# Performance work log

Measured on AMD Instinct MI355X. Metric: run time of the kernel, lower is better.

## Reference

```python
import jax, jax.numpy as jnp
import numpy as np
from jax import lax

BATCH = 2
COUNT = 5
OUT = 125


def _bins(n, out=OUT):
    # PyTorch adaptive_max_pool2d bin boundaries: start=floor(i*n/out), end=ceil((i+1)*n/out)
    i = np.arange(out)
    s = (i * n) // out
    e = -((-(i + 1) * n) // out)
    m = int((e - s).max())
    idx = s[:, None] + np.arange(m)[None, :]
    return np.minimum(idx, n - 1), idx < e[:, None]


def _apool(img):
    # adaptive max pool 2d of [H,W] -> [OUT,OUT]; H,W are concrete Python ints
    H, W = img.shape
    ri, rv = _bins(H)
    ci, cv = _bins(W)
    r = jnp.where(rv[:, :, None], img[ri], -jnp.inf).max(axis=1)       # [OUT, W]
    return jnp.where(cv[None], r[:, ci], -jnp.inf).max(axis=2)         # [OUT, OUT]


def _conv(x, w, b):
    y = lax.conv_general_dilated(x, w, (1, 1), 'VALID', dimension_numbers=('NCHW', 'OIHW', 'NCHW'))
    return y + b[None, :, None, None]


def _bn(x, g, be, m, v):
    inv = g * lax.rsqrt(v + 1e-5)
    return x * inv[None, :, None, None] + (be - m * inv)[None, :, None, None]


def _pool(x, k, s):
    return lax.reduce_window(x, -np.inf, lax.max, (1, 1, k, k), (1, 1, s, s), 'VALID')


def _forward(x, ROI, roi_layer, w1, b1, g1, be1, m1, v1, w2, b2, g2, be2, m2, v2,
             w3, b3, g3, be3, m3, v3, w4, b4, g4, be4, m4, v4, fw1, fb1, fw2, fb2, fw3, fb3):
    ROI = np.asarray(ROI)
    rl = int(roi_layer)
    roiX = jax.nn.relu(_bn(_conv(x, w1, b1), g1, be1, m1, v1))  # [2,3,252,252]
    crops = []
    for k in range(BATCH):
        xs = []
        for j in range(rl):
            for i in range(COUNT):
                y1, y2, x1, x2 = (int(v) for v in ROI[k, i, 0])
                y1 = int(y1 * 0.9); y2 = int(y2 * 0.9); x2 = int(x2 * 0.9); x1 = int(x1 * 0.9)
                xs.append(_apool(roiX[k, j, y1:y2, x1:x2]))
        crops.append(xs)
    # original code prepends each batch's crop list -> batch order reversed; .numpy() detaches grads
    xb = lax.stop_gradient(jnp.stack(crops[1] + crops[0]).reshape(BATCH, COUNT * rl, OUT, OUT))
    norX = _pool(jax.nn.relu(_bn(_conv(x, w2, b2), g2, be2, m2, v2)), 4, 2)  # [2,20,125,125]
    h = jnp.concatenate([norX, xb], axis=1)                                   # [2,35,125,125]
    h = _pool(jax.nn.relu(_bn(_conv(h, w3, b3), g3, be3, m3, v3)), 2, 2)      # [2,50,60,60]
    h = _pool(jax.nn.relu(_bn(_conv(h, w4, b4), g4, be4, m4, v4)), 2, 2)      # [2,25,28,28]
    h = h.reshape(BATCH, -1)                                                  # [2,19600]
    h = jax.nn.relu(h @ fw1 + fb1)
    h = jax.nn.relu(h @ fw2 + fb2)
    h = jax.nn.relu(h @ fw3 + fb3)
    return jax.nn.softmax(h, axis=1)


def setup_inputs() -> dict:
    key = jax.random.key(0)
    ks = jax.random.split(key, 8)
    rng = np.random.default_rng(0)
    y1 = rng.integers(0, 100, (BATCH, COUNT))
    y2 = np.minimum(y1 + rng.integers(60, 150, (BATCH, COUNT)), 251)
    x1 = rng.integers(0, 100, (BATCH, COUNT))
    x2 = np.minimum(x1 + rng.integers(60, 150, (BATCH, COUNT)), 251)
    ROI = jnp.asarray(np.stack([y1, y2, x1, x2], -1)[:, :, None, :].astype(np.int32))
    d = {'x': jax.random.normal(ks[0], (BATCH, 1, 256, 256), jnp.float32), 'ROI': ROI, 'roi_layer': 3}
    d.update(w1=jax.random.normal(ks[1], (3, 1, 5, 5)) * 0.05, b1=jnp.zeros(3), g1=jnp.ones(3), be1=jnp.zeros(3), m1=jnp.zeros(3), v1=jnp.ones(3))
    d.update(w2=jax.random.normal(ks[2], (20, 1, 5, 5)) * 0.05, b2=jnp.zeros(20), g2=jnp.ones(20), be2=jnp.zeros(20), m2=jnp.zeros(20), v2=jnp.ones(20))
    d.update(w3=jax.random.normal(ks[3], (50, 35, 5, 5)) * 0.05, b3=jnp.zeros(50), g3=jnp.ones(50), be3=jnp.zeros(50), m3=jnp.zeros(50), v3=jnp.ones(50))
    d.update(w4=jax.random.normal(ks[4], (25, 50, 5, 5)) * 0.05, b4=jnp.zeros(25), g4=jnp.ones(25), be4=jnp.zeros(25), m4=jnp.zeros(25), v4=jnp.ones(25))
    d.update(fw1=jax.random.normal(ks[5], (25 * 28 * 28, 1024)) * 0.01, fb1=jnp.zeros(1024),
             fw2=jax.random.normal(ks[6], (1024, 32)) * 0.05, fb2=jnp.zeros(32),
             fw3=jax.random.normal(ks[7], (32, 2)) * 0.05, fb3=jnp.zeros(2))
    return d


def reference(x, ROI, roi_layer, w1, b1, g1, be1, m1, v1, w2, b2, g2, be2, m2, v2,
              w3, b3, g3, be3, m3, v3, w4, b4, g4, be4, m4, v4, fw1, fb1, fw2, fb2, fw3, fb3):
    return _forward(x, ROI, roi_layer, w1, b1, g1, be1, m1, v1, w2, b2, g2, be2, m2, v2,
                    w3, b3, g3, be3, m3, v3, w4, b4, g4, be4, m4, v4, fw1, fb1, fw2, fb2, fw3, fb3)
```

## Files before the change

### kernel.cpp

```cpp
#include <hip/hip_runtime.h>
#include <math.h>


#define RL 3
#define NCH 35

__global__ __launch_bounds__(256) void conv2_roi(
    const float* __restrict__ x, const int* __restrict__ ROI,
    const float* __restrict__ w2, const float* __restrict__ b2, const float* __restrict__ g2,
    const float* __restrict__ be2, const float* __restrict__ m2, const float* __restrict__ v2,
    const float* __restrict__ w1, const float* __restrict__ b1, const float* __restrict__ g1,
    const float* __restrict__ be1, const float* __restrict__ m1, const float* __restrict__ v1,
    const float* __restrict__ w3, const float* __restrict__ w4,
    float* __restrict__ wp3, float* __restrict__ wp4,
    float* __restrict__ h1) {
    if (blockIdx.y >= 70) {
        const float* src = (blockIdx.y == 70) ? w3 : w4;
        float* dst = (blockIdx.y == 70) ? wp3 : wp4;
        int rows = (blockIdx.y == 70) ? 50 * 35 : 25 * 50;
        int total = rows * 28;
        for (int i = blockIdx.x * 256 + threadIdx.x; i < total; i += gridDim.x * 256) {
            int t = i % 28, r = i / 28;
            dst[i] = (t < 25) ? src[r * 25 + t] : 0.f;
        }
        return;
    }
    int i = blockIdx.x * 256 + threadIdx.x;
    if (i >= 125 * 125) return;
    int oy = i / 125, ox = i % 125;
    if (blockIdx.y < 40) {
        int c = blockIdx.y % 20;
        int bi = blockIdx.y / 20;
        const float* xp = x + bi * 256 * 256 + (2 * oy) * 256 + 2 * ox;
        float wl[25];
#pragma unroll
        for (int k = 0; k < 25; k++) wl[k] = w2[c * 25 + k];
        float in[8][8];
#pragma unroll
        for (int r = 0; r < 8; r++)
#pragma unroll
            for (int k = 0; k < 4; k++) {
                float2 v2v = *(const float2*)(xp + r * 256 + 2 * k);
                in[r][2 * k] = v2v.x;
                in[r][2 * k + 1] = v2v.y;
            }
        float inv = g2[c] * rsqrtf(v2[c] + 1e-5f);
        float sh = (b2[c] - m2[c]) * inv + be2[c];
        float mx = -INFINITY;
#pragma unroll
        for (int py = 0; py < 4; py++) {
#pragma unroll
            for (int px = 0; px < 4; px++) {
                float acc = 0.f;
#pragma unroll
                for (int ky = 0; ky < 5; ky++)
#pragma unroll
                    for (int kx = 0; kx < 5; kx++)
                        acc = fmaf(in[py + ky][px + kx], wl[ky * 5 + kx], acc);
                mx = fmaxf(mx, fmaxf(acc * inv + sh, 0.f));
            }
        }
        h1[((bi * NCH + c) * 125 + oy) * 125 + ox] = mx;
    } else {
        int yz = blockIdx.y - 40;
        int bi = yz / 15;
        int cc = yz % 15;
        int sb = 1 - bi;
        int j = cc / 5;
        int ri = cc % 5;
        const int* rp = ROI + (sb * 5 + ri) * 4;
        int y1 = (9 * rp[0]) / 10;
        int y2 = (9 * rp[1]) / 10;
        int x1 = (9 * rp[2]) / 10;
        int x2 = (9 * rp[3]) / 10;
        int H = y2 - y1;
        int W = x2 - x1;
        int sy = (oy * H) / 125, ey = ((oy + 1) * H + 124) / 125;
        int sx = (ox * W) / 125, ex = ((ox + 1) * W + 124) / 125;
        float wl[25];
#pragma unroll
        for (int k = 0; k < 25; k++) wl[k] = w1[j * 25 + k];
        float inv = g1[j] * rsqrtf(v1[j] + 1e-5f);
        float sh = (b1[j] - m1[j]) * inv + be1[j];
        const float* xp = x + sb * 256 * 256;
        float mx = -INFINITY;
        for (int r = sy; r < ey; r++) {
            for (int c2 = sx; c2 < ex; c2++) {
                int Y = y1 + r, X = x1 + c2;
                float acc = 0.f;
#pragma unroll
                for (int ky = 0; ky < 5; ky++)
#pragma unroll
                    for (int kx = 0; kx < 5; kx++)
                        acc = fmaf(xp[(Y + ky) * 256 + X + kx], wl[ky * 5 + kx], acc);
                mx = fmaxf(mx, fmaxf(acc * inv + sh, 0.f));
            }
        }
        h1[((bi * NCH + 20 + cc) * 125 + oy) * 125 + ox] = mx;
    }
}

template <int IW, int PO, int CI, int CO, int G, int NG, int NS, int BST, int CST>
__global__ __launch_bounds__(64, 4) void conv_partial(
    const float* __restrict__ in, const float* __restrict__ wp,
    float* __restrict__ pac) {
    static_assert(G == 2 || G == 3, "schedule supports G=2,3");
    __shared__ float tile[2][20][24];

    const int lane = threadIdx.x;
    const int sy = lane >> 3, sx = lane & 7;
    int z = blockIdx.z;
    const int ng = z % NG; z /= NG;
    const int s = z % NS;
    const int bi = z / NS;
    const int co0 = ng * G;
    constexpr int CPS = (CI + NS - 1) / NS;
    const int ci0 = s * CPS;
    const int ci1 = (ci0 + CPS < CI) ? ci0 + CPS : CI;
    const int px0 = (8 * (int)blockIdx.x < PO - 8) ? 8 * (int)blockIdx.x : PO - 8;
    const int py0 = (8 * (int)blockIdx.y < PO - 8) ? 8 * (int)blockIdx.y : PO - 8;
    const int px = px0 + sx, py = py0 + sy;
    const float* ip = in + (size_t)bi * BST + (size_t)(2 * py0) * IW + 2 * px0;

    int cw[G];
#pragma unroll
    for (int gg = 0; gg < G; gg++) cw[gg] = (co0 + gg < CO) ? co0 + gg : CO - 1;

    float2 sreg[4];
    auto loadstage = [&](int ci) {
        const float* src = ip + (size_t)ci * CST;
#pragma unroll
        for (int k = 0; k < 4; k++) {
            int p = lane + k * 64;
            if (p < 200) {
                int r = p / 10, c2 = (p % 10) * 2;
                sreg[k] = *(const float2*)(src + r * IW + c2);
            }
        }
    };
    auto writestage = [&](int buf) {
#pragma unroll
        for (int k = 0; k < 4; k++) {
            int p = lane + k * 64;
            if (p < 200) {
                int r = p / 10, c2 = (p % 10) * 2;
                *(float2*)&tile[buf][r][c2] = sreg[k];
            }
        }
    };

    float4 wA[7], wB[7];
    auto wload = [&](float4(&wr)[7], int gg, int ci) {
        const float* src = wp + ((size_t)cw[gg] * CI + ci) * 28;
#pragma unroll
        for (int k = 0; k < 7; k++) wr[k] = *(const float4*)(src + 4 * k);
    };

    float acc[G][4];
#pragma unroll
    for (int gg = 0; gg < G; gg++)
#pragma unroll
        for (int q = 0; q < 4; q++) acc[gg][q] = 0.f;

#define WE(W, t) ((t) % 4 == 0 ? W[(t) / 4].x : (t) % 4 == 1 ? W[(t) / 4].y : (t) % 4 == 2 ? W[(t) / 4].z : W[(t) / 4].w)
#define FMAG(W, gg)                                                            \
    {                                                                          \
        _Pragma("unroll") for (int ky = 0; ky < 5; ky++) {                     \
            _Pragma("unroll") for (int kx = 0; kx < 5; kx++) {                 \
                float wv = WE(W, ky * 5 + kx);                                 \
                float e00 = ((kx)&1) ? p[ky][kx >> 1].y : p[ky][kx >> 1].x;    \
                float e01 = ((kx + 1) & 1) ? p[ky][(kx + 1) >> 1].y : p[ky][(kx + 1) >> 1].x; \
                float e10 = ((kx)&1) ? p[ky + 1][kx >> 1].y : p[ky + 1][kx >> 1].x; \
                float e11 = ((kx + 1) & 1) ? p[ky + 1][(kx + 1) >> 1].y : p[ky + 1][(kx + 1) >> 1].x; \
                acc[gg][0] = fmaf(e00, wv, acc[gg][0]);                        \
                acc[gg][1] = fmaf(e01, wv, acc[gg][1]);                        \
                acc[gg][2] = fmaf(e10, wv, acc[gg][2]);                        \
                acc[gg][3] = fmaf(e11, wv, acc[gg][3]);                        \
            }                                                                  \
        }                                                                      \
    }

    loadstage(ci0);
    writestage(0);

    for (int ci = ci0; ci < ci1; ci++) {
        const int cur = (ci - ci0) & 1;
        if (ci + 1 < ci1) loadstage(ci + 1);
        wload(wA, 0, ci);
        float2 p[6][3];
#pragma unroll
        for (int r = 0; r < 6; r++)
#pragma unroll
            for (int c = 0; c < 3; c++)
                p[r][c] = *(const float2*)&tile[cur][2 * sy + r][2 * sx + 2 * c];
        wload(wB, 1, ci);
        FMAG(wA, 0);
        if constexpr (G == 3) {
            wload(wA, 2, ci);
            FMAG(wB, 1);
            FMAG(wA, 2);
        } else {
            FMAG(wB, 1);
        }
        if (ci + 1 < ci1) writestage(cur ^ 1);
    }
#undef FMAG
#undef WE

    constexpr int CW = 2 * PO;
#pragma unroll
    for (int gg = 0; gg < G; gg++) {
        int co = co0 + gg;
        if (co < CO) {
            size_t base = (((size_t)(s * 2 + bi) * CO + co) * CW + 2 * py) * CW + 2 * px;
            float2 r0 = {acc[gg][0], acc[gg][1]};
            float2 r1 = {acc[gg][2], acc[gg][3]};
            *(float2*)&pac[base] = r0;
            *(float2*)&pac[base + CW] = r1;
        }
    }
}

template <int PO, int CO, int INIT>
__global__ __launch_bounds__(256) void conv_finish(
    const float* __restrict__ pac,
    const float* __restrict__ b, const float* __restrict__ g,
    const float* __restrict__ be, const float* __restrict__ m,
    const float* __restrict__ v, float* __restrict__ out,
    const float* __restrict__ fb1, float* __restrict__ fc1o) {
    int idx = blockIdx.x * 256 + threadIdx.x;
    if (INIT && idx < 2048) fc1o[idx] = fb1[idx & 1023];
    int total = 2 * CO * PO * PO;
    if (idx >= total) return;
    int px = idx % PO;
    int t = idx / PO;
    int py = t % PO; t /= PO;
    int co = t % CO;
    int bi = t / CO;
    constexpr int CW = 2 * PO;
    constexpr size_t SS = (size_t)2 * CO * CW * CW;
    size_t base = (((size_t)bi * CO + co) * CW + 2 * py) * CW + 2 * px;
    float s00 = 0.f, s01 = 0.f, s10 = 0.f, s11 = 0.f;
#pragma unroll
    for (int s = 0; s < 4; s++) {
        float2 a0 = *(const float2*)&pac[base + s * SS];
        float2 a1 = *(const float2*)&pac[base + s * SS + CW];
        s00 += a0.x; s01 += a0.y; s10 += a1.x; s11 += a1.y;
    }
    float inv = g[co] * rsqrtf(v[co] + 1e-5f);
    float sh = (b[co] - m[co]) * inv + be[co];
    float q0 = fmaxf(s00 * inv + sh, 0.f);
    float q1 = fmaxf(s01 * inv + sh, 0.f);
    float q2 = fmaxf(s10 * inv + sh, 0.f);
    float q3 = fmaxf(s11 * inv + sh, 0.f);
    out[idx] = fmaxf(fmaxf(q0, q1), fmaxf(q2, q3));
}

#define CHUNK 50
__global__ void fc1_mm(const float* __restrict__ pac,
                       const float* __restrict__ b4, const float* __restrict__ g4,
                       const float* __restrict__ be4, const float* __restrict__ m4,
                       const float* __restrict__ v4,
                       const float* __restrict__ w, float* __restrict__ out) {
    __shared__ float sh[2][CHUNK];
    int o = blockIdx.x * 256 + threadIdx.x;
    int i0 = blockIdx.y * CHUNK;
    if (threadIdx.x < 2 * CHUNK) {
        int r = threadIdx.x / CHUNK, t = threadIdx.x % CHUNK;
        int e = i0 + t;
        int px = e % 28;
        int t2 = e / 28;
        int py = t2 % 28;
        int co = t2 / 28;
        const int CW = 56;
        const int SS = 2 * 25 * CW * CW;
        int base = ((r * 25 + co) * CW + 2 * py) * CW + 2 * px;
        float s00 = 0.f, s01 = 0.f, s10 = 0.f, s11 = 0.f;
#pragma unroll
        for (int s = 0; s < 4; s++) {
            float2 a0 = *(const float2*)&pac[base + s * SS];
            float2 a1 = *(const float2*)&pac[base + s * SS + CW];
            s00 += a0.x; s01 += a0.y; s10 += a1.x; s11 += a1.y;
        }
        float inv = g4[co] * rsqrtf(v4[co] + 1e-5f);
        float shv = (b4[co] - m4[co]) * inv + be4[co];
        float q0 = fmaxf(s00 * inv + shv, 0.f);
        float q1 = fmaxf(s01 * inv + shv, 0.f);
        float q2 = fmaxf(s10 * inv + shv, 0.f);
        float q3 = fmaxf(s11 * inv + shv, 0.f);
        sh[r][t] = fmaxf(fmaxf(q0, q1), fmaxf(q2, q3));
    }
    __syncthreads();
    float a0 = 0.f, a1 = 0.f;
    const float* wp = w + (size_t)i0 * 1024 + o;
#pragma unroll
    for (int i = 0; i < CHUNK; i++) {
        float wv = wp[(size_t)i * 1024];
        a0 = fmaf(sh[0][i], wv, a0);
        a1 = fmaf(sh[1][i], wv, a1);
    }
    atomicAdd(&out[o], a0);
    atomicAdd(&out[1024 + o], a1);
}

__global__ void head(const float* __restrict__ fc1o, const float* __restrict__ fw2,
                     const float* __restrict__ fb2, const float* __restrict__ fw3,
                     const float* __restrict__ fb3, float* __restrict__ out) {
    int bi = blockIdx.x;
    __shared__ float h[1024];
    __shared__ float red[256];
    __shared__ float s2[32];
    for (int i = threadIdx.x; i < 1024; i += 256) h[i] = fmaxf(fc1o[bi * 1024 + i], 0.f);
    __syncthreads();
    int o = threadIdx.x >> 3;
    int part = threadIdx.x & 7;
    float a = 0.f;
    for (int i = part * 128; i < part * 128 + 128; i++) a += h[i] * fw2[i * 32 + o];
    red[threadIdx.x] = a;
    __syncthreads();
    if (part == 0) {
        float s = 0.f;
        for (int p = 0; p < 8; p++) s += red[(o << 3) + p];
        s2[o] = fmaxf(s + fb2[o], 0.f);
    }
    __syncthreads();
    if (threadIdx.x == 0) {
        float z0 = fb3[0], z1 = fb3[1];
        for (int i = 0; i < 32; i++) {
            z0 += s2[i] * fw3[i * 2];
            z1 += s2[i] * fw3[i * 2 + 1];
        }
        z0 = fmaxf(z0, 0.f);
        z1 = fmaxf(z1, 0.f);
        float mx = fmaxf(z0, z1);
        float e0 = expf(z0 - mx), e1 = expf(z1 - mx);
        float s = e0 + e1;
        out[bi * 2 + 0] = e0 / s;
        out[bi * 2 + 1] = e1 / s;
    }
}

extern "C" void kernel_launch(void* const* d_in, const int* in_sizes, int n_in,
                              void* d_out, int out_size, void* d_ws, size_t ws_size,
                              hipStream_t stream) {
    const float* x   = (const float*)d_in[0];
    const int*   ROI = (const int*)d_in[1];
    const float* w1 = (const float*)d_in[3];
    const float* b1 = (const float*)d_in[4];
    const float* g1 = (const float*)d_in[5];
    const float* be1 = (const float*)d_in[6];
    const float* m1 = (const float*)d_in[7];
    const float* v1 = (const float*)d_in[8];
    const float* w2 = (const float*)d_in[9];
    const float* b2 = (const float*)d_in[10];
    const float* g2 = (const float*)d_in[11];
    const float* be2 = (const float*)d_in[12];
    const float* m2 = (const float*)d_in[13];
    const float* v2 = (const float*)d_in[14];
    const float* w3 = (const float*)d_in[15];
    const float* b3 = (const float*)d_in[16];
    const float* g3 = (const float*)d_in[17];
    const float* be3 = (const float*)d_in[18];
    const float* m3 = (const float*)d_in[19];
    const float* v3 = (const float*)d_in[20];
    const float* w4 = (const float*)d_in[21];
    const float* b4 = (const float*)d_in[22];
    const float* g4 = (const float*)d_in[23];
    const float* be4 = (const float*)d_in[24];
    const float* m4 = (const float*)d_in[25];
    const float* v4 = (const float*)d_in[26];
    const float* fw1 = (const float*)d_in[27];
    const float* fb1 = (const float*)d_in[28];
    const float* fw2 = (const float*)d_in[29];
    const float* fb2 = (const float*)d_in[30];
    const float* fw3 = (const float*)d_in[31];
    const float* fb3 = (const float*)d_in[32];
    float* out = (float*)d_out;

    float* ws = (float*)d_ws;
    float* h1   = ws;
    float* p3   = h1 + 1093750;
    float* fc1o = p3 + 360000;
    float* pac3 = fc1o + 2048;
    float* pac4 = pac3;
    float* wp3  = pac3 + 5760000;
    float* wp4  = wp3 + 49000;

    {
        dim3 grd((125 * 125 + 255) / 256, 72);
        conv2_roi<<<grd, 256, 0, stream>>>(x, ROI, w2, b2, g2, be2, m2, v2,
                                           w1, b1, g1, be1, m1, v1,
                                           w3, w4, wp3, wp4, h1);
    }
    {
        dim3 grd(8, 8, 2 * 4 * 17);
        conv_partial<125, 60, NCH, 50, 3, 17, 4, 35 * 15625, 15625>
            <<<grd, 64, 0, stream>>>(h1, wp3, pac3);
    }
    {
        int total = 2 * 50 * 60 * 60;
        conv_finish<60, 50, 1><<<(total + 255) / 256, 256, 0, stream>>>(
            pac3, b3, g3, be3, m3, v3, p3, fb1, fc1o);
    }
    {
        dim3 grd(4, 4, 2 * 4 * 13);
        conv_partial<60, 28, 50, 25, 2, 13, 4, 180000, 3600>
            <<<grd, 64, 0, stream>>>(p3, wp4, pac4);
    }
    {
        dim3 grd(4, 392);
        fc1_mm<<<grd, 256, 0, stream>>>(pac4, b4, g4, be4, m4, v4, fw1, fc1o);
    }
    head<<<2, 256, 0, stream>>>(fc1o, fw2, fb2, fw3, fb3, out);
}
```

Before: 118.8 us.

## Fuse MLP head into fc1 via last-block counter and vectorize fc1 loads

The separate head kernel is folded into fc1_mm. The last block to finish, found with an atomic counter that conv_finish resets, runs the fc2/fc3/softmax tail, which saves one kernel launch. fc1 is reworked so that each block covers 28 input rows across all 1024 outputs, reading weights as float4, with 700 blocks in place of a 4x392 grid. The conv_partial loop also moves the shared-memory stage write earlier so it overlaps the FMAs. The costs are more atomics per thread and a serialized tail in one block.

Result: slower. 246.8 us (+107.8%).

```diff
diff --git a/kernel.cpp b/kernel.cpp
--- a/kernel.cpp
+++ b/kernel.cpp
@@ -198,11 +198,12 @@
         if constexpr (G == 3) {
             wload(wA, 2, ci);
             FMAG(wB, 1);
+            if (ci + 1 < ci1) writestage(cur ^ 1);
             FMAG(wA, 2);
         } else {
+            if (ci + 1 < ci1) writestage(cur ^ 1);
             FMAG(wB, 1);
         }
-        if (ci + 1 < ci1) writestage(cur ^ 1);
     }
 #undef FMAG
 #undef WE
@@ -227,9 +228,10 @@
     const float* __restrict__ b, const float* __restrict__ g,
     const float* __restrict__ be, const float* __restrict__ m,
     const float* __restrict__ v, float* __restrict__ out,
-    const float* __restrict__ fb1, float* __restrict__ fc1o) {
+    const float* __restrict__ fb1, float* __restrict__ fc1o, int* __restrict__ cnt) {
     int idx = blockIdx.x * 256 + threadIdx.x;
     if (INIT && idx < 2048) fc1o[idx] = fb1[idx & 1023];
+    if (INIT && idx == 2048) *cnt = 0;
     int total = 2 * CO * PO * PO;
     if (idx >= total) return;
     int px = idx % PO;
@@ -256,17 +258,26 @@
     out[idx] = fmaxf(fmaxf(q0, q1), fmaxf(q2, q3));
 }
 
-#define CHUNK 50
-__global__ void fc1_mm(const float* __restrict__ pac,
-                       const float* __restrict__ b4, const float* __restrict__ g4,
-                       const float* __restrict__ be4, const float* __restrict__ m4,
-                       const float* __restrict__ v4,
-                       const float* __restrict__ w, float* __restrict__ out) {
+#define CHUNK 28
+#define NCHK 700
+__global__ __launch_bounds__(256) void fc1_mm(
+    const float* __restrict__ pac,
+    const float* __restrict__ b4, const float* __restrict__ g4,
+    const float* __restrict__ be4, const float* __restrict__ m4,
+    const float* __restrict__ v4,
+    const float* __restrict__ w, float* __restrict__ fc1o, int* __restrict__ cnt,
+    const float* __restrict__ fw2, const float* __restrict__ fb2,
+    const float* __restrict__ fw3, const float* __restrict__ fb3,
+    float* __restrict__ out) {
     __shared__ float sh[2][CHUNK];
-    int o = blockIdx.x * 256 + threadIdx.x;
-    int i0 = blockIdx.y * CHUNK;
-    if (threadIdx.x < 2 * CHUNK) {
-        int r = threadIdx.x / CHUNK, t = threadIdx.x % CHUNK;
+    __shared__ float hh[1024];
+    __shared__ float red[256];
+    __shared__ float s2v[32];
+    __shared__ int lastf;
+    const int tid = threadIdx.x;
+    const int i0 = blockIdx.x * CHUNK;
+    if (tid < 2 * CHUNK) {
+        int r = tid / CHUNK, t = tid % CHUNK;
         int e = i0 + t;
         int px = e % 28;
         int t2 = e / 28;
@@ -291,52 +302,67 @@
         sh[r][t] = fmaxf(fmaxf(q0, q1), fmaxf(q2, q3));
     }
     __syncthreads();
-    float a0 = 0.f, a1 = 0.f;
-    const float* wp = w + (size_t)i0 * 1024 + o;
-#pragma unroll
+    const int o4 = tid * 4;
+    float4 a0 = {0.f, 0.f, 0.f, 0.f}, a1 = {0.f, 0.f, 0.f, 0.f};
+    const float* wp = w + (size_t)i0 * 1024 + o4;
+#pragma unroll 4
     for (int i = 0; i < CHUNK; i++) {
-        float wv = wp[(size_t)i * 1024];
-        a0 = fmaf(sh[0][i], wv, a0);
-        a1 = fmaf(sh[1][i], wv, a1);
-    }
-    atomicAdd(&out[o], a0);
-    atomicAdd(&out[1024 + o], a1);
-}
-
-__global__ void head(const float* __restrict__ fc1o, const float* __restrict__ fw2,
-                     const float* __restrict__ fb2, const float* __restrict__ fw3,
-                     const float* __restrict__ fb3, float* __restrict__ out) {
-    int bi = blockIdx.x;
-    __shared__ float h[1024];
-    __shared__ float red[256];
-    __shared__ float s2[32];
-    for (int i = threadIdx.x; i < 1024; i += 256) h[i] = fmaxf(fc1o[bi * 1024 + i], 0.f);
+        float4 wv = *(const float4*)(wp + (size_t)i * 1024);
+        float h0 = sh[0][i], h1v = sh[1][i];
+        a0.x = fmaf(h0, wv.x, a0.x);
+        a0.y = fmaf(h0, wv.y, a0.y);
+        a0.z = fmaf(h0, wv.z, a0.z);
+        a0.w = fmaf(h0, wv.w, a0.w);
+        a1.x = fmaf(h1v, wv.x, a1.x);
+        a1.y = fmaf(h1v, wv.y, a1.y);
+        a1.z = fmaf(h1v, wv.z, a1.z);
+        a1.w = fmaf(h1v, wv.w, a1.w);
+    }
+    atomicAdd(&fc1o[o4 + 0], a0.x);
+    atomicAdd(&fc1o[o4 + 1], a0.y);
+    atomicAdd(&fc1o[o4 + 2], a0.z);
+    atomicAdd(&fc1o[o4 + 3], a0.w);
+    atomicAdd(&fc1o[1024 + o4 + 0], a1.x);
+    atomicAdd(&fc1o[1024 + o4 + 1], a1.y);
+    atomicAdd(&fc1o[1024 + o4 + 2], a1.z);
+    atomicAdd(&fc1o[1024 + o4 + 3], a1.w);
+
+    __threadfence();
     __syncthreads();
-    int o = threadIdx.x >> 3;
-    int part = threadIdx.x & 7;
-    float a = 0.f;
-    for (int i = part * 128; i < part * 128 + 128; i++) a += h[i] * fw2[i * 32 + o];
-    red[threadIdx.x] = a;
+    if (tid == 0) lastf = (atomicAdd(cnt, 1) == NCHK - 1) ? 1 : 0;
     __syncthreads();
-    if (part == 0) {
-        float s = 0.f;
-        for (int p = 0; p < 8; p++) s += red[(o << 3) + p];
-        s2[o] = fmaxf(s + fb2[o], 0.f);
-    }
-    __syncthreads();
-    if (threadIdx.x == 0) {
-        float z0 = fb3[0], z1 = fb3[1];
-        for (int i = 0; i < 32; i++) {
-            z0 += s2[i] * fw3[i * 2];
-            z1 += s2[i] * fw3[i * 2 + 1];
-        }
-        z0 = fmaxf(z0, 0.f);
-        z1 = fmaxf(z1, 0.f);
-        float mx = fmaxf(z0, z1);
-        float e0 = expf(z0 - mx), e1 = expf(z1 - mx);
-        float s = e0 + e1;
-        out[bi * 2 + 0] = e0 / s;
-        out[bi * 2 + 1] = e1 / s;
+    if (!lastf) return;
+    for (int bi = 0; bi < 2; bi++) {
+        for (int i = tid; i < 1024; i += 256)
+            hh[i] = fmaxf(atomicAdd(&fc1o[bi * 1024 + i], 0.f), 0.f);
+        __syncthreads();
+        int o = tid >> 3;
+        int part = tid & 7;
+        float a = 0.f;
+        for (int i = part * 128; i < part * 128 + 128; i++) a += hh[i] * fw2[i * 32 + o];
+        red[tid] = a;
+        __syncthreads();
+        if (part == 0) {
+            float s = 0.f;
+            for (int p = 0; p < 8; p++) s += red[(o << 3) + p];
+            s2v[o] = fmaxf(s + fb2[o], 0.f);
+        }
+        __syncthreads();
+        if (tid == 0) {
+            float z0 = fb3[0], z1 = fb3[1];
+            for (int i = 0; i < 32; i++) {
+                z0 += s2v[i] * fw3[i * 2];
+                z1 += s2v[i] * fw3[i * 2 + 1];
+            }
+            z0 = fmaxf(z0, 0.f);
+            z1 = fmaxf(z1, 0.f);
+            float mx = fmaxf(z0, z1);
+            float e0 = expf(z0 - mx), e1 = expf(z1 - mx);
+            float s = e0 + e1;
+            out[bi * 2 + 0] = e0 / s;
+            out[bi * 2 + 1] = e1 / s;
+        }
+        __syncthreads();
     }
 }
 
@@ -385,6 +411,7 @@
     float* pac4 = pac3;
     float* wp3  = pac3 + 5760000;
     float* wp4  = wp3 + 49000;
+    int*   cnt  = (int*)(wp4 + 35000);
 
     {
         dim3 grd((125 * 125 + 255) / 256, 72);
@@ -400,7 +427,7 @@
     {
         int total = 2 * 50 * 60 * 60;
         conv_finish<60, 50, 1><<<(total + 255) / 256, 256, 0, stream>>>(
-            pac3, b3, g3, be3, m3, v3, p3, fb1, fc1o);
+            pac3, b3, g3, be3, m3, v3, p3, fb1, fc1o, cnt);
     }
     {
         dim3 grd(4, 4, 2 * 4 * 13);
@@ -408,8 +435,7 @@
             <<<grd, 64, 0, stream>>>(p3, wp4, pac4);
     }
     {
-        dim3 grd(4, 392);
-        fc1_mm<<<grd, 256, 0, stream>>>(pac4, b4, g4, be4, m4, v4, fw1, fc1o);
-    }
-    head<<<2, 256, 0, stream>>>(fc1o, fw2, fb2, fw3, fb3, out);
+        fc1_mm<<<NCHK, 256, 0, stream>>>(pac4, b4, g4, be4, m4, v4, fw1, fc1o,
+                                         cnt, fw2, fb2, fw3, fb3, out);
+    }
 }
```
